# Kernel optimization log

Hardware: AMD Instinct MI355X
Metric: run time of the kernel (lower is better)

Reference implementation:

```python
import jax, jax.numpy as jnp
import numpy as np

B, N, M, K = 8, 4096, 1024, 16   # clouds, points/cloud, fps samples/cloud (ratio=0.25), max neighbors
R = 0.3                          # radius
C_IN, H1, H2, C_OUT = 3, 64, 64, 128


def setup_inputs() -> dict:
    key = jax.random.key(0)
    ks = jax.random.split(key, 6)
    pos = jax.random.normal(ks[0], (B * N, 3), jnp.float32)
    x = jax.random.normal(ks[1], (B * N, C_IN), jnp.float32)
    batch = jnp.repeat(jnp.arange(B, dtype=jnp.int32), N)
    def lin(k, fan_in, fan_out):
        return jax.random.normal(k, (fan_in, fan_out), jnp.float32) / np.float32(np.sqrt(fan_in))
    W1 = lin(ks[2], C_IN + 3, H1); b1 = jnp.zeros((H1,), jnp.float32)
    W2 = lin(ks[3], H1, H2);       b2 = jnp.zeros((H2,), jnp.float32)
    W3 = lin(ks[4], H2, C_OUT);    b3 = jnp.zeros((C_OUT,), jnp.float32)
    return dict(x=x, pos=pos, batch=batch, W1=W1, b1=b1, W2=W2, b2=b2, W3=W3, b3=b3)


def _fps(pos_b):
    # farthest point sampling for one cloud: [N,3] -> [M] indices (start at point 0)
    d0 = jnp.sum((pos_b - pos_b[0]) ** 2, axis=-1)
    def body(d, _):
        i = jnp.argmax(d).astype(jnp.int32)
        d = jnp.minimum(d, jnp.sum((pos_b - pos_b[i]) ** 2, axis=-1))
        return d, i
    _, idxs = jax.lax.scan(body, d0, None, length=M - 1)
    return jnp.concatenate([jnp.zeros((1,), jnp.int32), idxs])


def _radius(pos_s_b, pos_b):
    # for each of M query points, first-K (by index) points within R: -> neigh [M,K], mask [M,K]
    d2 = jnp.sum((pos_s_b[:, None, :] - pos_b[None, :, :]) ** 2, axis=-1)  # [M,N]
    valid = d2 <= R * R
    keyed = jnp.where(valid, jnp.arange(N, dtype=jnp.int32)[None, :], N)
    first = jnp.sort(keyed, axis=1)[:, :K]
    mask = first < N
    return jnp.where(mask, first, 0), mask


def reference(x, pos, batch, W1, b1, W2, b2, W3, b3):
    posB = pos.reshape(B, N, 3)
    xB = x.reshape(B, N, C_IN)

    idx = jax.vmap(_fps)(posB)                                       # [B,M]
    pos_s = jnp.take_along_axis(posB, idx[..., None], axis=1)        # [B,M,3]

    neigh, mask = jax.vmap(_radius)(pos_s, posB)                     # [B,M,K]

    # flat (global) indices, matching PyG's concatenated-batch indexing
    src_flat = jnp.arange(B, dtype=jnp.int32)[:, None, None] * N + neigh            # [B,M,K]
    dst_flat = jnp.arange(B, dtype=jnp.int32)[:, None] * M + jnp.arange(M, dtype=jnp.int32)[None, :]  # [B,M]
    # PointConv(add_self_loops=True): remove_self_loops on numeric equality, then add (i,i)
    mask = mask & (src_flat != dst_flat[..., None])

    gather = jax.vmap(lambda a, nb: a[nb])
    x_j = gather(xB, neigh)                                          # [B,M,K,C_IN]
    pos_j = gather(posB, neigh)                                      # [B,M,K,3]
    rel = pos_j - pos_s[:, :, None, :]

    # self-loop edges: source point index i == target index i in flat indexing
    i_self = dst_flat.reshape(-1)                                    # [B*M]
    x_self = x[i_self]                                               # [B*M,C_IN]
    rel_self = pos[i_self] - pos_s.reshape(-1, 3)

    f_rad = jnp.concatenate([x_j, rel], axis=-1)                     # [B,M,K,6]
    f_self = jnp.concatenate([x_self, rel_self], axis=-1).reshape(B, M, 1, C_IN + 3)
    feats = jnp.concatenate([f_rad, f_self], axis=2)                 # [B,M,K+1,6]
    m_all = jnp.concatenate([mask, jnp.ones((B, M, 1), bool)], axis=2)

    h = jax.nn.relu(feats @ W1 + b1)
    h = jax.nn.relu(h @ W2 + b2)
    h = h @ W3 + b3                                                  # [B,M,K+1,C_OUT]
    h = jnp.where(m_all[..., None], h, -jnp.inf)
    out = jnp.max(h, axis=2).reshape(B * M, C_OUT)                   # max aggregation

    batch_s = jnp.repeat(jnp.arange(B, dtype=batch.dtype), M)
    return out, pos_s.reshape(B * M, 3), batch_s
```

## Files before the change

### kernel.cpp

```cpp
#include <hip/hip_runtime.h>
#include <hip/hip_bf16.h>
#include <math.h>

constexpr int BB   = 8;
constexpr int NN   = 4096;
constexpr int MM   = 1024;
constexpr int KK   = 16;
constexpr int COUT = 128;
#define RSQ 0.09f

__device__ __forceinline__ float dist2_exact(float ax, float ay, float az,
                                             float bx, float by, float bz) {
    float dx = __fsub_rn(ax, bx);
    float dy = __fsub_rn(ay, by);
    float dz = __fsub_rn(az, bz);
    return __fadd_rn(__fadd_rn(__fmul_rn(dx, dx), __fmul_rn(dy, dy)), __fmul_rn(dz, dz));
}

template<int CTRL>
__device__ __forceinline__ unsigned dpp_mov_u(unsigned v) {
    return (unsigned)__builtin_amdgcn_update_dpp((int)v, (int)v, CTRL, 0xF, 0xF, false);
}
__device__ __forceinline__ float readlane_f(float v, int j) {
    return __int_as_float(__builtin_amdgcn_readlane(__float_as_int(v), j));
}
__device__ __forceinline__ unsigned umax2(unsigned a, unsigned b) { return a > b ? a : b; }
__device__ __forceinline__ unsigned umin2(unsigned a, unsigned b) { return a < b ? a : b; }

__global__ __launch_bounds__(256, 1) void fps_kernel(const float* __restrict__ pos,
                                                     float* __restrict__ pos_s,
                                                     float* __restrict__ batch_s) {
    const int b    = blockIdx.x;
    const int tid  = threadIdx.x;
    const int lane = tid & 63;
    const int wave = tid >> 6;
    const float* pb = pos + (size_t)b * NN * 3;

    __shared__ float4 spos[NN];
    __shared__ int    shist[MM];
    __shared__ unsigned long long slotK[2][4];

    for (int i = tid; i < NN; i += 256)
        spos[i] = make_float4(pb[i * 3 + 0], pb[i * 3 + 1], pb[i * 3 + 2], 0.0f);
    for (int i = tid; i < MM; i += 256)
        batch_s[(size_t)b * MM + i] = (float)b;
    if (tid == 0) shist[0] = 0;
    if (tid < 8) slotK[tid >> 2][tid & 3] = 0ull;
    __syncthreads();

    float px[16], py[16], pz[16], d[16];
    const float4 p0 = spos[0];
#pragma unroll
    for (int k = 0; k < 16; k++) {
        float4 pt = spos[tid + k * 256];
        px[k] = pt.x; py[k] = pt.y; pz[k] = pt.z;
        d[k] = dist2_exact(pt.x, pt.y, pt.z, p0.x, p0.y, p0.z);
    }
    float bv;
    {
        float t1[8], t2[4];
#pragma unroll
        for (int k = 0; k < 8; k++) t1[k] = fmaxf(d[2 * k], d[2 * k + 1]);
#pragma unroll
        for (int k = 0; k < 4; k++) t2[k] = fmaxf(t1[2 * k], t1[2 * k + 1]);
        bv = fmaxf(fmaxf(t2[0], t2[1]), fmaxf(t2[2], t2[3]));
    }

    for (int m = 1; m < MM; m++) {
        const int par = m & 1;
        const unsigned tagm = (unsigned)m;

        const unsigned bvb = __float_as_uint(bv);

        unsigned rv = bvb;
        rv = umax2(rv, dpp_mov_u<0x111>(rv));
        rv = umax2(rv, dpp_mov_u<0x112>(rv));
        rv = umax2(rv, dpp_mov_u<0x114>(rv));
        rv = umax2(rv, dpp_mov_u<0x118>(rv));
        const unsigned r0 = (unsigned)__builtin_amdgcn_readlane((int)rv, 15);
        const unsigned r1 = (unsigned)__builtin_amdgcn_readlane((int)rv, 31);
        const unsigned r2 = (unsigned)__builtin_amdgcn_readlane((int)rv, 47);
        const unsigned r3 = (unsigned)__builtin_amdgcn_readlane((int)rv, 63);
        const unsigned vstar = umax2(umax2(r0, r1), umax2(r2, r3));

        unsigned kmask = 0u;
#pragma unroll
        for (int k = 0; k < 16; k++)
            kmask |= (d[k] == bv) ? (1u << k) : 0u;
        const unsigned bi = (unsigned)(tid + (__builtin_ctz(kmask) << 8));

        unsigned cand = (bvb == vstar) ? bi : 0xFFFFFFFFu;
        cand = umin2(cand, dpp_mov_u<0x111>(cand));
        cand = umin2(cand, dpp_mov_u<0x112>(cand));
        cand = umin2(cand, dpp_mov_u<0x114>(cand));
        cand = umin2(cand, dpp_mov_u<0x118>(cand));
        const unsigned c0 = (unsigned)__builtin_amdgcn_readlane((int)cand, 15);
        const unsigned c1 = (unsigned)__builtin_amdgcn_readlane((int)cand, 31);
        const unsigned c2 = (unsigned)__builtin_amdgcn_readlane((int)cand, 47);
        const unsigned c3 = (unsigned)__builtin_amdgcn_readlane((int)cand, 63);
        const unsigned wcand = umin2(umin2(c0, c1), umin2(c2, c3));

        if (lane == 0) {
            const unsigned long long key =
                ((unsigned long long)vstar << 32)
                | (unsigned long long)(((4095u - wcand) << 10) | tagm);
            __hip_atomic_store(&slotK[par][wave], key, __ATOMIC_RELAXED,
                               __HIP_MEMORY_SCOPE_WORKGROUP);
        }

        unsigned long long k0, k1, k2, k3;
        for (;;) {
            k0 = __hip_atomic_load(&slotK[par][0], __ATOMIC_RELAXED, __HIP_MEMORY_SCOPE_WORKGROUP);
            k1 = __hip_atomic_load(&slotK[par][1], __ATOMIC_RELAXED, __HIP_MEMORY_SCOPE_WORKGROUP);
            k2 = __hip_atomic_load(&slotK[par][2], __ATOMIC_RELAXED, __HIP_MEMORY_SCOPE_WORKGROUP);
            k3 = __hip_atomic_load(&slotK[par][3], __ATOMIC_RELAXED, __HIP_MEMORY_SCOPE_WORKGROUP);
            bool ok = (((unsigned)k0 & 1023u) == tagm) &
                      (((unsigned)k1 & 1023u) == tagm) &
                      (((unsigned)k2 & 1023u) == tagm) &
                      (((unsigned)k3 & 1023u) == tagm);
            if (ok) break;
        }

        unsigned long long kA = (k0 > k1) ? k0 : k1;
        unsigned long long kB = (k2 > k3) ? k2 : k3;
        unsigned long long kk = (kA > kB) ? kA : kB;
        const int fi = 4095 - (int)(((unsigned)kk >> 10) & 4095u);

        if (tid == 0) shist[m] = fi;

        const float4 sp = spos[fi];
        if (m < MM - 1) {
#pragma unroll
            for (int k = 0; k < 16; k++) {
                float nd = dist2_exact(px[k], py[k], pz[k], sp.x, sp.y, sp.z);
                d[k] = fminf(d[k], nd);
            }
            float t1[8], t2[4];
#pragma unroll
            for (int k = 0; k < 8; k++) t1[k] = fmaxf(d[2 * k], d[2 * k + 1]);
#pragma unroll
            for (int k = 0; k < 4; k++) t2[k] = fmaxf(t1[2 * k], t1[2 * k + 1]);
            bv = fmaxf(fmaxf(t2[0], t2[1]), fmaxf(t2[2], t2[3]));
        }
    }

    __syncthreads();
    for (int i = tid; i < MM; i += 256) {
        float4 sp = spos[shist[i]];
        size_t o = (size_t)b * MM + i;
        pos_s[o * 3 + 0] = sp.x;
        pos_s[o * 3 + 1] = sp.y;
        pos_s[o * 3 + 2] = sp.z;
    }
}

__global__ __launch_bounds__(256, 1) void radius_mlp_kernel(const float* __restrict__ x,
                                                            const float* __restrict__ pos,
                                                            const float* __restrict__ pos_s,
                                                            const float* __restrict__ W1,
                                                            const float* __restrict__ b1,
                                                            const float* __restrict__ W2,
                                                            const float* __restrict__ b2,
                                                            const float* __restrict__ W3,
                                                            const float* __restrict__ b3,
                                                            float* __restrict__ out) {
    __shared__ float sW2[64 * 64];
    __shared__ float sW3[64 * 128];
    __shared__ int   nslot[4][16];

    const int tid  = threadIdx.x;
    const int lane = tid & 63;
    const int wave = tid >> 6;

    {
        const float4* s2 = (const float4*)W2;
        float4*       d2 = (float4*)sW2;
        for (int i = tid; i < 64 * 64 / 4; i += 256) d2[i] = s2[i];
        const float4* s3 = (const float4*)W3;
        float4*       d3 = (float4*)sW3;
        for (int i = tid; i < 64 * 128 / 4; i += 256) d3[i] = s3[i];
    }
    float w1c[6];
#pragma unroll
    for (int c = 0; c < 6; c++) w1c[c] = W1[c * 64 + lane];
    const float bb1  = b1[lane];
    const float bb2  = b2[lane];
    const float bb3a = b3[lane];
    const float bb3b = b3[64 + lane];
    __syncthreads();

    const int q = blockIdx.x * 4 + wave;
    const int b = q >> 10;
    const float qx = pos_s[q * 3 + 0];
    const float qy = pos_s[q * 3 + 1];
    const float qz = pos_s[q * 3 + 2];

    if (lane < 16) nslot[wave][lane] = 0;
    const float* pb = pos + (size_t)b * NN * 3;
    int cnt = 0;
    for (int c = 0; c < NN / 64; c++) {
        int p = c * 64 + lane;
        float px = pb[p * 3 + 0], py = pb[p * 3 + 1], pz = pb[p * 3 + 2];
        float d2 = dist2_exact(qx, qy, qz, px, py, pz);
        bool val = (d2 <= RSQ);
        unsigned long long msk = __ballot(val);
        if (val) {
            int rank = __popcll(msk & ((1ull << lane) - 1ull));
            int slot = cnt + rank;
            if (slot < KK) nslot[wave][slot] = p;
        }
        cnt += __popcll(msk);
        if (cnt >= KK) break;
    }
    const int cnt16 = min(cnt, KK);

    const int4 n0 = *(const int4*)&nslot[wave][0];
    const int4 n1 = *(const int4*)&nslot[wave][4];
    const int4 n2 = *(const int4*)&nslot[wave][8];
    const int4 n3 = *(const int4*)&nslot[wave][12];
    const int nidx[16] = { n0.x, n0.y, n0.z, n0.w, n1.x, n1.y, n1.z, n1.w,
                           n2.x, n2.y, n2.z, n2.w, n3.x, n3.y, n3.z, n3.w };

    float h[17];
    unsigned vmask = 1u << 16;
#pragma unroll
    for (int e = 0; e < 16; e++) {
        const int p = (e < cnt16) ? nidx[e] : 0;
        const int g = b * NN + p;
        if ((e < cnt16) && (g != q)) vmask |= (1u << e);
        const float f0 = x[(size_t)g * 3 + 0];
        const float f1 = x[(size_t)g * 3 + 1];
        const float f2 = x[(size_t)g * 3 + 2];
        const float f3 = pos[(size_t)g * 3 + 0] - qx;
        const float f4 = pos[(size_t)g * 3 + 1] - qy;
        const float f5 = pos[(size_t)g * 3 + 2] - qz;
        float t = bb1 + f0 * w1c[0] + f1 * w1c[1] + f2 * w1c[2]
                      + f3 * w1c[3] + f4 * w1c[4] + f5 * w1c[5];
        h[e] = fmaxf(t, 0.0f);
    }
    {
        const int g = q;
        const float f0 = x[(size_t)g * 3 + 0];
        const float f1 = x[(size_t)g * 3 + 1];
        const float f2 = x[(size_t)g * 3 + 2];
        const float f3 = pos[(size_t)g * 3 + 0] - qx;
        const float f4 = pos[(size_t)g * 3 + 1] - qy;
        const float f5 = pos[(size_t)g * 3 + 2] - qz;
        float t = bb1 + f0 * w1c[0] + f1 * w1c[1] + f2 * w1c[2]
                      + f3 * w1c[3] + f4 * w1c[4] + f5 * w1c[5];
        h[16] = fmaxf(t, 0.0f);
    }

    float acc[17];
#pragma unroll
    for (int e = 0; e < 17; e++) acc[e] = bb2;
#pragma unroll 2
    for (int j = 0; j < 64; j++) {
        const float wj = sW2[j * 64 + lane];
#pragma unroll
        for (int e = 0; e < 17; e++) {
            const float hj = readlane_f(h[e], j);
            acc[e] = __builtin_fmaf(hj, wj, acc[e]);
        }
    }
#pragma unroll
    for (int e = 0; e < 17; e++) h[e] = fmaxf(acc[e], 0.0f);

    float a0[17], a1[17];
#pragma unroll
    for (int e = 0; e < 17; e++) { a0[e] = bb3a; a1[e] = bb3b; }
#pragma unroll 2
    for (int j = 0; j < 64; j++) {
        const float wa = sW3[j * 128 + lane];
        const float wb = sW3[j * 128 + 64 + lane];
#pragma unroll
        for (int e = 0; e < 17; e++) {
            const float hj = readlane_f(h[e], j);
            a0[e] = __builtin_fmaf(hj, wa, a0[e]);
            a1[e] = __builtin_fmaf(hj, wb, a1[e]);
        }
    }

    float m0 = -INFINITY, m1 = -INFINITY;
#pragma unroll
    for (int e = 0; e < 17; e++) {
        const bool v = (vmask >> e) & 1u;
        m0 = v ? fmaxf(m0, a0[e]) : m0;
        m1 = v ? fmaxf(m1, a1[e]) : m1;
    }
    out[(size_t)q * COUT + lane]      = m0;
    out[(size_t)q * COUT + 64 + lane] = m1;
}

extern "C" void kernel_launch(void* const* d_in, const int* in_sizes, int n_in,
                              void* d_out, int out_size, void* d_ws, size_t ws_size,
                              hipStream_t stream) {
    const float* x   = (const float*)d_in[0];
    const float* pos = (const float*)d_in[1];
    const float* W1 = (const float*)d_in[3];
    const float* b1 = (const float*)d_in[4];
    const float* W2 = (const float*)d_in[5];
    const float* b2 = (const float*)d_in[6];
    const float* W3 = (const float*)d_in[7];
    const float* b3 = (const float*)d_in[8];

    float* outF    = (float*)d_out;
    float* out     = outF;
    float* pos_s   = outF + (size_t)BB * MM * COUT;
    float* batch_s = pos_s + (size_t)BB * MM * 3;

    fps_kernel<<<BB, 256, 0, stream>>>(pos, pos_s, batch_s);
    radius_mlp_kernel<<<BB * MM / 4, 256, 0, stream>>>(x, pos, pos_s,
                                                       W1, b1, W2, b2, W3, b3, out);
}
```

Before: 895.3 us.

## Fuse FPS and radius-MLP into one persistent kernel with flag-based streaming

Merges the two kernels into a single launch of 256 blocks. 8 blocks run farthest point sampling and publish each selected index to a global flag array, while the other 248 blocks poll those flags and start the radius search and MLP for each sample as soon as it appears. The aim is to overlap the serial FPS loop with the neighbour and MLP work instead of running them back to back. It adds a memset, spin-polling on global memory, and a guard counter that could give up early. It also relies on all blocks being co-resident, and the polling traffic may slow the FPS blocks.

```diff
diff --git a/kernel.cpp b/kernel.cpp
--- a/kernel.cpp
+++ b/kernel.cpp
@@ -7,6 +7,7 @@
 constexpr int MM   = 1024;
 constexpr int KK   = 16;
 constexpr int COUT = 128;
+constexpr int NWRK = 992;
 #define RSQ 0.09f
 
 __device__ __forceinline__ float dist2_exact(float ax, float ay, float az,
@@ -27,114 +28,55 @@
 __device__ __forceinline__ unsigned umax2(unsigned a, unsigned b) { return a > b ? a : b; }
 __device__ __forceinline__ unsigned umin2(unsigned a, unsigned b) { return a < b ? a : b; }
 
-__global__ __launch_bounds__(256, 1) void fps_kernel(const float* __restrict__ pos,
-                                                     float* __restrict__ pos_s,
-                                                     float* __restrict__ batch_s) {
-    const int b    = blockIdx.x;
+__global__ __launch_bounds__(256, 1) void fused_kernel(const float* __restrict__ x,
+                                                       const float* __restrict__ pos,
+                                                       const float* __restrict__ W1,
+                                                       const float* __restrict__ b1,
+                                                       const float* __restrict__ W2,
+                                                       const float* __restrict__ b2,
+                                                       const float* __restrict__ W3,
+                                                       const float* __restrict__ b3,
+                                                       unsigned* __restrict__ gsel,
+                                                       float* __restrict__ out,
+                                                       float* __restrict__ pos_s,
+                                                       float* __restrict__ batch_s) {
+    __shared__ float4 spos[NN];
+    __shared__ int    shist[MM];
+    __shared__ unsigned long long slotK[2][4];
+    __shared__ float sW2[64 * 64];
+    __shared__ float sW3[64 * 128];
+    __shared__ int   nslot[4][16];
+
     const int tid  = threadIdx.x;
     const int lane = tid & 63;
     const int wave = tid >> 6;
-    const float* pb = pos + (size_t)b * NN * 3;
-
-    __shared__ float4 spos[NN];
-    __shared__ int    shist[MM];
-    __shared__ unsigned long long slotK[2][4];
-
-    for (int i = tid; i < NN; i += 256)
-        spos[i] = make_float4(pb[i * 3 + 0], pb[i * 3 + 1], pb[i * 3 + 2], 0.0f);
-    for (int i = tid; i < MM; i += 256)
-        batch_s[(size_t)b * MM + i] = (float)b;
-    if (tid == 0) shist[0] = 0;
-    if (tid < 8) slotK[tid >> 2][tid & 3] = 0ull;
-    __syncthreads();
-
-    float px[16], py[16], pz[16], d[16];
-    const float4 p0 = spos[0];
-#pragma unroll
-    for (int k = 0; k < 16; k++) {
-        float4 pt = spos[tid + k * 256];
-        px[k] = pt.x; py[k] = pt.y; pz[k] = pt.z;
-        d[k] = dist2_exact(pt.x, pt.y, pt.z, p0.x, p0.y, p0.z);
-    }
-    float bv;
-    {
-        float t1[8], t2[4];
-#pragma unroll
-        for (int k = 0; k < 8; k++) t1[k] = fmaxf(d[2 * k], d[2 * k + 1]);
-#pragma unroll
-        for (int k = 0; k < 4; k++) t2[k] = fmaxf(t1[2 * k], t1[2 * k + 1]);
-        bv = fmaxf(fmaxf(t2[0], t2[1]), fmaxf(t2[2], t2[3]));
-    }
-
-    for (int m = 1; m < MM; m++) {
-        const int par = m & 1;
-        const unsigned tagm = (unsigned)m;
-
-        const unsigned bvb = __float_as_uint(bv);
-
-        unsigned rv = bvb;
-        rv = umax2(rv, dpp_mov_u<0x111>(rv));
-        rv = umax2(rv, dpp_mov_u<0x112>(rv));
-        rv = umax2(rv, dpp_mov_u<0x114>(rv));
-        rv = umax2(rv, dpp_mov_u<0x118>(rv));
-        const unsigned r0 = (unsigned)__builtin_amdgcn_readlane((int)rv, 15);
-        const unsigned r1 = (unsigned)__builtin_amdgcn_readlane((int)rv, 31);
-        const unsigned r2 = (unsigned)__builtin_amdgcn_readlane((int)rv, 47);
-        const unsigned r3 = (unsigned)__builtin_amdgcn_readlane((int)rv, 63);
-        const unsigned vstar = umax2(umax2(r0, r1), umax2(r2, r3));
-
-        unsigned kmask = 0u;
-#pragma unroll
-        for (int k = 0; k < 16; k++)
-            kmask |= (d[k] == bv) ? (1u << k) : 0u;
-        const unsigned bi = (unsigned)(tid + (__builtin_ctz(kmask) << 8));
-
-        unsigned cand = (bvb == vstar) ? bi : 0xFFFFFFFFu;
-        cand = umin2(cand, dpp_mov_u<0x111>(cand));
-        cand = umin2(cand, dpp_mov_u<0x112>(cand));
-        cand = umin2(cand, dpp_mov_u<0x114>(cand));
-        cand = umin2(cand, dpp_mov_u<0x118>(cand));
-        const unsigned c0 = (unsigned)__builtin_amdgcn_readlane((int)cand, 15);
-        const unsigned c1 = (unsigned)__builtin_amdgcn_readlane((int)cand, 31);
-        const unsigned c2 = (unsigned)__builtin_amdgcn_readlane((int)cand, 47);
-        const unsigned c3 = (unsigned)__builtin_amdgcn_readlane((int)cand, 63);
-        const unsigned wcand = umin2(umin2(c0, c1), umin2(c2, c3));
-
-        if (lane == 0) {
-            const unsigned long long key =
-                ((unsigned long long)vstar << 32)
-                | (unsigned long long)(((4095u - wcand) << 10) | tagm);
-            __hip_atomic_store(&slotK[par][wave], key, __ATOMIC_RELAXED,
-                               __HIP_MEMORY_SCOPE_WORKGROUP);
-        }
-
-        unsigned long long k0, k1, k2, k3;
-        for (;;) {
-            k0 = __hip_atomic_load(&slotK[par][0], __ATOMIC_RELAXED, __HIP_MEMORY_SCOPE_WORKGROUP);
-            k1 = __hip_atomic_load(&slotK[par][1], __ATOMIC_RELAXED, __HIP_MEMORY_SCOPE_WORKGROUP);
-            k2 = __hip_atomic_load(&slotK[par][2], __ATOMIC_RELAXED, __HIP_MEMORY_SCOPE_WORKGROUP);
-            k3 = __hip_atomic_load(&slotK[par][3], __ATOMIC_RELAXED, __HIP_MEMORY_SCOPE_WORKGROUP);
-            bool ok = (((unsigned)k0 & 1023u) == tagm) &
-                      (((unsigned)k1 & 1023u) == tagm) &
-                      (((unsigned)k2 & 1023u) == tagm) &
-                      (((unsigned)k3 & 1023u) == tagm);
-            if (ok) break;
-        }
-
-        unsigned long long kA = (k0 > k1) ? k0 : k1;
-        unsigned long long kB = (k2 > k3) ? k2 : k3;
-        unsigned long long kk = (kA > kB) ? kA : kB;
-        const int fi = 4095 - (int)(((unsigned)kk >> 10) & 4095u);
-
-        if (tid == 0) shist[m] = fi;
-
-        const float4 sp = spos[fi];
-        if (m < MM - 1) {
-#pragma unroll
-            for (int k = 0; k < 16; k++) {
-                float nd = dist2_exact(px[k], py[k], pz[k], sp.x, sp.y, sp.z);
-                d[k] = fminf(d[k], nd);
-            }
+
+    if (blockIdx.x < BB) {
+        const int b = blockIdx.x;
+        const float* pb = pos + (size_t)b * NN * 3;
+
+        for (int i = tid; i < NN; i += 256)
+            spos[i] = make_float4(pb[i * 3 + 0], pb[i * 3 + 1], pb[i * 3 + 2], 0.0f);
+        for (int i = tid; i < MM; i += 256)
+            batch_s[(size_t)b * MM + i] = (float)b;
+        if (tid == 0) {
+            shist[0] = 0;
+            __hip_atomic_store(&gsel[(size_t)b * MM], 1u, __ATOMIC_RELAXED,
+                               __HIP_MEMORY_SCOPE_AGENT);
+        }
+        if (tid < 8) slotK[tid >> 2][tid & 3] = 0ull;
+        __syncthreads();
+
+        float px[16], py[16], pz[16], d[16];
+        const float4 p0 = spos[0];
+#pragma unroll
+        for (int k = 0; k < 16; k++) {
+            float4 pt = spos[tid + k * 256];
+            px[k] = pt.x; py[k] = pt.y; pz[k] = pt.z;
+            d[k] = dist2_exact(pt.x, pt.y, pt.z, p0.x, p0.y, p0.z);
+        }
+        float bv;
+        {
             float t1[8], t2[4];
 #pragma unroll
             for (int k = 0; k < 8; k++) t1[k] = fmaxf(d[2 * k], d[2 * k + 1]);
@@ -142,35 +84,99 @@
             for (int k = 0; k < 4; k++) t2[k] = fmaxf(t1[2 * k], t1[2 * k + 1]);
             bv = fmaxf(fmaxf(t2[0], t2[1]), fmaxf(t2[2], t2[3]));
         }
+
+        for (int m = 1; m < MM; m++) {
+            const int par = m & 1;
+            const unsigned tagm = (unsigned)m;
+
+            const unsigned bvb = __float_as_uint(bv);
+
+            unsigned rv = bvb;
+            rv = umax2(rv, dpp_mov_u<0x111>(rv));
+            rv = umax2(rv, dpp_mov_u<0x112>(rv));
+            rv = umax2(rv, dpp_mov_u<0x114>(rv));
+            rv = umax2(rv, dpp_mov_u<0x118>(rv));
+            const unsigned r0 = (unsigned)__builtin_amdgcn_readlane((int)rv, 15);
+            const unsigned r1 = (unsigned)__builtin_amdgcn_readlane((int)rv, 31);
+            const unsigned r2 = (unsigned)__builtin_amdgcn_readlane((int)rv, 47);
+            const unsigned r3 = (unsigned)__builtin_amdgcn_readlane((int)rv, 63);
+            const unsigned vstar = umax2(umax2(r0, r1), umax2(r2, r3));
+
+            unsigned kmask = 0u;
+#pragma unroll
+            for (int k = 0; k < 16; k++)
+                kmask |= (d[k] == bv) ? (1u << k) : 0u;
+            const unsigned bi = (unsigned)(tid + (__builtin_ctz(kmask) << 8));
+
+            unsigned cand = (bvb == vstar) ? bi : 0xFFFFFFFFu;
+            cand = umin2(cand, dpp_mov_u<0x111>(cand));
+            cand = umin2(cand, dpp_mov_u<0x112>(cand));
+            cand = umin2(cand, dpp_mov_u<0x114>(cand));
+            cand = umin2(cand, dpp_mov_u<0x118>(cand));
+            const unsigned c0 = (unsigned)__builtin_amdgcn_readlane((int)cand, 15);
+            const unsigned c1 = (unsigned)__builtin_amdgcn_readlane((int)cand, 31);
+            const unsigned c2 = (unsigned)__builtin_amdgcn_readlane((int)cand, 47);
+            const unsigned c3 = (unsigned)__builtin_amdgcn_readlane((int)cand, 63);
+            const unsigned wcand = umin2(umin2(c0, c1), umin2(c2, c3));
+
+            if (lane == 0) {
+                const unsigned long long key =
+                    ((unsigned long long)vstar << 32)
+                    | (unsigned long long)(((4095u - wcand) << 10) | tagm);
+                __hip_atomic_store(&slotK[par][wave], key, __ATOMIC_RELAXED,
+                                   __HIP_MEMORY_SCOPE_WORKGROUP);
+            }
+
+            unsigned long long k0, k1, k2, k3;
+            for (;;) {
+                k0 = __hip_atomic_load(&slotK[par][0], __ATOMIC_RELAXED, __HIP_MEMORY_SCOPE_WORKGROUP);
+                k1 = __hip_atomic_load(&slotK[par][1], __ATOMIC_RELAXED, __HIP_MEMORY_SCOPE_WORKGROUP);
+                k2 = __hip_atomic_load(&slotK[par][2], __ATOMIC_RELAXED, __HIP_MEMORY_SCOPE_WORKGROUP);
+                k3 = __hip_atomic_load(&slotK[par][3], __ATOMIC_RELAXED, __HIP_MEMORY_SCOPE_WORKGROUP);
+                bool ok = (((unsigned)k0 & 1023u) == tagm) &
+                          (((unsigned)k1 & 1023u) == tagm) &
+                          (((unsigned)k2 & 1023u) == tagm) &
+                          (((unsigned)k3 & 1023u) == tagm);
+                if (ok) break;
+            }
+
+            unsigned long long kA = (k0 > k1) ? k0 : k1;
+            unsigned long long kB = (k2 > k3) ? k2 : k3;
+            unsigned long long kk = (kA > kB) ? kA : kB;
+            const int fi = 4095 - (int)(((unsigned)kk >> 10) & 4095u);
+
+            if (tid == 0) {
+                shist[m] = fi;
+                __hip_atomic_store(&gsel[(size_t)b * MM + m], (unsigned)(fi + 1),
+                                   __ATOMIC_RELAXED, __HIP_MEMORY_SCOPE_AGENT);
+            }
+
+            const float4 sp = spos[fi];
+            if (m < MM - 1) {
+#pragma unroll
+                for (int k = 0; k < 16; k++) {
+                    float nd = dist2_exact(px[k], py[k], pz[k], sp.x, sp.y, sp.z);
+                    d[k] = fminf(d[k], nd);
+                }
+                float t1[8], t2[4];
+#pragma unroll
+                for (int k = 0; k < 8; k++) t1[k] = fmaxf(d[2 * k], d[2 * k + 1]);
+#pragma unroll
+                for (int k = 0; k < 4; k++) t2[k] = fmaxf(t1[2 * k], t1[2 * k + 1]);
+                bv = fmaxf(fmaxf(t2[0], t2[1]), fmaxf(t2[2], t2[3]));
+            }
+        }
+
+        __syncthreads();
+        for (int i = tid; i < MM; i += 256) {
+            float4 sp = spos[shist[i]];
+            size_t o = (size_t)b * MM + i;
+            pos_s[o * 3 + 0] = sp.x;
+            pos_s[o * 3 + 1] = sp.y;
+            pos_s[o * 3 + 2] = sp.z;
+        }
+        return;
     }
-
-    __syncthreads();
-    for (int i = tid; i < MM; i += 256) {
-        float4 sp = spos[shist[i]];
-        size_t o = (size_t)b * MM + i;
-        pos_s[o * 3 + 0] = sp.x;
-        pos_s[o * 3 + 1] = sp.y;
-        pos_s[o * 3 + 2] = sp.z;
-    }
-}
-
-__global__ __launch_bounds__(256, 1) void radius_mlp_kernel(const float* __restrict__ x,
-                                                            const float* __restrict__ pos,
-                                                            const float* __restrict__ pos_s,
-                                                            const float* __restrict__ W1,
-                                                            const float* __restrict__ b1,
-                                                            const float* __restrict__ W2,
-                                                            const float* __restrict__ b2,
-                                                            const float* __restrict__ W3,
-                                                            const float* __restrict__ b3,
-                                                            float* __restrict__ out) {
-    __shared__ float sW2[64 * 64];
-    __shared__ float sW3[64 * 128];
-    __shared__ int   nslot[4][16];
-
-    const int tid  = threadIdx.x;
-    const int lane = tid & 63;
-    const int wave = tid >> 6;
 
     {
         const float4* s2 = (const float4*)W2;
@@ -189,107 +195,128 @@
     const float bb3b = b3[64 + lane];
     __syncthreads();
 
-    const int q = blockIdx.x * 4 + wave;
-    const int b = q >> 10;
-    const float qx = pos_s[q * 3 + 0];
-    const float qy = pos_s[q * 3 + 1];
-    const float qz = pos_s[q * 3 + 2];
-
-    if (lane < 16) nslot[wave][lane] = 0;
-    const float* pb = pos + (size_t)b * NN * 3;
-    int cnt = 0;
-    for (int c = 0; c < NN / 64; c++) {
-        int p = c * 64 + lane;
-        float px = pb[p * 3 + 0], py = pb[p * 3 + 1], pz = pb[p * 3 + 2];
-        float d2 = dist2_exact(qx, qy, qz, px, py, pz);
-        bool val = (d2 <= RSQ);
-        unsigned long long msk = __ballot(val);
-        if (val) {
-            int rank = __popcll(msk & ((1ull << lane) - 1ull));
-            int slot = cnt + rank;
-            if (slot < KK) nslot[wave][slot] = p;
-        }
-        cnt += __popcll(msk);
-        if (cnt >= KK) break;
+    const int W = (blockIdx.x - BB) * 4 + wave;
+
+    unsigned todo = 0u;
+#pragma unroll
+    for (int k = 0; k < 9; k++)
+        if (W + NWRK * k < BB * MM) todo |= (1u << k);
+
+    int guard = 0;
+    while (todo) {
+        if (++guard > 200000) break;
+#pragma unroll
+        for (int k = 0; k < 9; k++) {
+            if (!((todo >> k) & 1u)) continue;
+            const int q = W + NWRK * k;
+            const unsigned v = __hip_atomic_load(&gsel[q], __ATOMIC_RELAXED,
+                                                 __HIP_MEMORY_SCOPE_AGENT);
+            if (v == 0u || v > (unsigned)NN) continue;
+            todo &= ~(1u << k);
+
+            const int b  = q >> 10;
+            const int fi = (int)v - 1;
+            const float qx = pos[((size_t)b * NN + fi) * 3 + 0];
+            const float qy = pos[((size_t)b * NN + fi) * 3 + 1];
+            const float qz = pos[((size_t)b * NN + fi) * 3 + 2];
+
+            if (lane < 16) nslot[wave][lane] = 0;
+            const float* pb = pos + (size_t)b * NN * 3;
+            int cnt = 0;
+            for (int c = 0; c < NN / 64; c++) {
+                int p = c * 64 + lane;
+                float px = pb[p * 3 + 0], py = pb[p * 3 + 1], pz = pb[p * 3 + 2];
+                float d2 = dist2_exact(qx, qy, qz, px, py, pz);
+                bool val = (d2 <= RSQ);
+                unsigned long long msk = __ballot(val);
+                if (val) {
+                    int rank = __popcll(msk & ((1ull << lane) - 1ull));
+                    int slot = cnt + rank;
+                    if (slot < KK) nslot[wave][slot] = p;
+                }
+                cnt += __popcll(msk);
+                if (cnt >= KK) break;
+            }
+            const int cnt16 = min(cnt, KK);
+
+            const int4 n0 = *(const int4*)&nslot[wave][0];
+            const int4 n1 = *(const int4*)&nslot[wave][4];
+            const int4 n2 = *(const int4*)&nslot[wave][8];
+            const int4 n3 = *(const int4*)&nslot[wave][12];
+            const int nidx[16] = { n0.x, n0.y, n0.z, n0.w, n1.x, n1.y, n1.z, n1.w,
+                                   n2.x, n2.y, n2.z, n2.w, n3.x, n3.y, n3.z, n3.w };
+
+            float h[17];
+            unsigned vmask = 1u << 16;
+#pragma unroll
+            for (int e = 0; e < 16; e++) {
+                const int p = (e < cnt16) ? nidx[e] : 0;
+                const int g = b * NN + p;
+                if ((e < cnt16) && (g != q)) vmask |= (1u << e);
+                const float f0 = x[(size_t)g * 3 + 0];
+                const float f1 = x[(size_t)g * 3 + 1];
+                const float f2 = x[(size_t)g * 3 + 2];
+                const float f3 = pos[(size_t)g * 3 + 0] - qx;
+                const float f4 = pos[(size_t)g * 3 + 1] - qy;
+                const float f5 = pos[(size_t)g * 3 + 2] - qz;
+                float t = bb1 + f0 * w1c[0] + f1 * w1c[1] + f2 * w1c[2]
+                              + f3 * w1c[3] + f4 * w1c[4] + f5 * w1c[5];
+                h[e] = fmaxf(t, 0.0f);
+            }
+            {
+                const int g = q;
+                const float f0 = x[(size_t)g * 3 + 0];
+                const float f1 = x[(size_t)g * 3 + 1];
+                const float f2 = x[(size_t)g * 3 + 2];
+                const float f3 = pos[(size_t)g * 3 + 0] - qx;
+                const float f4 = pos[(size_t)g * 3 + 1] - qy;
+                const float f5 = pos[(size_t)g * 3 + 2] - qz;
+                float t = bb1 + f0 * w1c[0] + f1 * w1c[1] + f2 * w1c[2]
+                              + f3 * w1c[3] + f4 * w1c[4] + f5 * w1c[5];
+                h[16] = fmaxf(t, 0.0f);
+            }
+
+            float acc[17];
+#pragma unroll
+            for (int e = 0; e < 17; e++) acc[e] = bb2;
+#pragma unroll 2
+            for (int j = 0; j < 64; j++) {
+                const float wj = sW2[j * 64 + lane];
+#pragma unroll
+                for (int e = 0; e < 17; e++) {
+                    const float hj = readlane_f(h[e], j);
+                    acc[e] = __builtin_fmaf(hj, wj, acc[e]);
+                }
+            }
+#pragma unroll
+            for (int e = 0; e < 17; e++) h[e] = fmaxf(acc[e], 0.0f);
+
+            float a0[17], a1[17];
+#pragma unroll
+            for (int e = 0; e < 17; e++) { a0[e] = bb3a; a1[e] = bb3b; }
+#pragma unroll 2
+            for (int j = 0; j < 64; j++) {
+                const float wa = sW3[j * 128 + lane];
+                const float wb = sW3[j * 128 + 64 + lane];
+#pragma unroll
+                for (int e = 0; e < 17; e++) {
+                    const float hj = readlane_f(h[e], j);
+                    a0[e] = __builtin_fmaf(hj, wa, a0[e]);
+                    a1[e] = __builtin_fmaf(hj, wb, a1[e]);
+                }
+            }
+
+            float m0 = -INFINITY, m1 = -INFINITY;
+#pragma unroll
+            for (int e = 0; e < 17; e++) {
+                const bool vv = (vmask >> e) & 1u;
+                m0 = vv ? fmaxf(m0, a0[e]) : m0;
+                m1 = vv ? fmaxf(m1, a1[e]) : m1;
+            }
+            out[(size_t)q * COUT + lane]      = m0;
+            out[(size_t)q * COUT + 64 + lane] = m1;
+        }
     }
-    const int cnt16 = min(cnt, KK);
-
-    const int4 n0 = *(const int4*)&nslot[wave][0];
-    const int4 n1 = *(const int4*)&nslot[wave][4];
-    const int4 n2 = *(const int4*)&nslot[wave][8];
-    const int4 n3 = *(const int4*)&nslot[wave][12];
-    const int nidx[16] = { n0.x, n0.y, n0.z, n0.w, n1.x, n1.y, n1.z, n1.w,
-                           n2.x, n2.y, n2.z, n2.w, n3.x, n3.y, n3.z, n3.w };
-
-    float h[17];
-    unsigned vmask = 1u << 16;
-#pragma unroll
-    for (int e = 0; e < 16; e++) {
-        const int p = (e < cnt16) ? nidx[e] : 0;
-        const int g = b * NN + p;
-        if ((e < cnt16) && (g != q)) vmask |= (1u << e);
-        const float f0 = x[(size_t)g * 3 + 0];
-        const float f1 = x[(size_t)g * 3 + 1];
-        const float f2 = x[(size_t)g * 3 + 2];
-        const float f3 = pos[(size_t)g * 3 + 0] - qx;
-        const float f4 = pos[(size_t)g * 3 + 1] - qy;
-        const float f5 = pos[(size_t)g * 3 + 2] - qz;
-        float t = bb1 + f0 * w1c[0] + f1 * w1c[1] + f2 * w1c[2]
-                      + f3 * w1c[3] + f4 * w1c[4] + f5 * w1c[5];
-        h[e] = fmaxf(t, 0.0f);
-    }
-    {
-        const int g = q;
-        const float f0 = x[(size_t)g * 3 + 0];
-        const float f1 = x[(size_t)g * 3 + 1];
-        const float f2 = x[(size_t)g * 3 + 2];
-        const float f3 = pos[(size_t)g * 3 + 0] - qx;
-        const float f4 = pos[(size_t)g * 3 + 1] - qy;
-        const float f5 = pos[(size_t)g * 3 + 2] - qz;
-        float t = bb1 + f0 * w1c[0] + f1 * w1c[1] + f2 * w1c[2]
-                      + f3 * w1c[3] + f4 * w1c[4] + f5 * w1c[5];
-        h[16] = fmaxf(t, 0.0f);
-    }
-
-    float acc[17];
-#pragma unroll
-    for (int e = 0; e < 17; e++) acc[e] = bb2;
-#pragma unroll 2
-    for (int j = 0; j < 64; j++) {
-        const float wj = sW2[j * 64 + lane];
-#pragma unroll
-        for (int e = 0; e < 17; e++) {
-            const float hj = readlane_f(h[e], j);
-            acc[e] = __builtin_fmaf(hj, wj, acc[e]);
-        }
-    }
-#pragma unroll
-    for (int e = 0; e < 17; e++) h[e] = fmaxf(acc[e], 0.0f);
-
-    float a0[17], a1[17];
-#pragma unroll
-    for (int e = 0; e < 17; e++) { a0[e] = bb3a; a1[e] = bb3b; }
-#pragma unroll 2
-    for (int j = 0; j < 64; j++) {
-        const float wa = sW3[j * 128 + lane];
-        const float wb = sW3[j * 128 + 64 + lane];
-#pragma unroll
-        for (int e = 0; e < 17; e++) {
-            const float hj = readlane_f(h[e], j);
-            a0[e] = __builtin_fmaf(hj, wa, a0[e]);
-            a1[e] = __builtin_fmaf(hj, wb, a1[e]);
-        }
-    }
-
-    float m0 = -INFINITY, m1 = -INFINITY;
-#pragma unroll
-    for (int e = 0; e < 17; e++) {
-        const bool v = (vmask >> e) & 1u;
-        m0 = v ? fmaxf(m0, a0[e]) : m0;
-        m1 = v ? fmaxf(m1, a1[e]) : m1;
-    }
-    out[(size_t)q * COUT + lane]      = m0;
-    out[(size_t)q * COUT + 64 + lane] = m1;
 }
 
 extern "C" void kernel_launch(void* const* d_in, const int* in_sizes, int n_in,
@@ -309,7 +336,10 @@
     float* pos_s   = outF + (size_t)BB * MM * COUT;
     float* batch_s = pos_s + (size_t)BB * MM * 3;
 
-    fps_kernel<<<BB, 256, 0, stream>>>(pos, pos_s, batch_s);
-    radius_mlp_kernel<<<BB * MM / 4, 256, 0, stream>>>(x, pos, pos_s,
-                                                       W1, b1, W2, b2, W3, b3, out);
-}
+    unsigned* gsel = (unsigned*)d_ws;
+
+    hipMemsetAsync(gsel, 0, (size_t)BB * MM * sizeof(unsigned), stream);
+
+    fused_kernel<<<256, 256, 0, stream>>>(x, pos, W1, b1, W2, b2, W3, b3,
+                                          gsel, out, pos_s, batch_s);
+}
```

Result: faster. 826.7 us (-7.7%).
